# Kernel optimization log

Hardware: AMD Instinct MI355X
Metric: run time of the kernel (lower is better)

Reference implementation:

```python
import jax, jax.numpy as jnp
import numpy as np

B, NQ, NKV = 16, 4096, 77
QUERY_DIM, CONTEXT_DIM = 320, 768
HEADS, DIM_HEAD = 8, 64
INNER = HEADS * DIM_HEAD
SCALE = DIM_HEAD ** (-0.5)
MAX_NEG = -jnp.finfo(jnp.float32).max / 2


def setup_inputs() -> dict:
    key = jax.random.key(0)
    ks = jax.random.split(key, 8)
    x = jax.random.normal(ks[0], (B, NQ, QUERY_DIM), dtype=jnp.float32)
    context = jax.random.normal(ks[1], (B, NKV, CONTEXT_DIM), dtype=jnp.float32)
    mask = jax.random.randint(ks[2], (B, 1, 1, NKV), 0, 2).astype(bool)
    s = 0.02
    Wq = jax.random.normal(ks[3], (QUERY_DIM, INNER), dtype=jnp.float32) * s
    Wk = jax.random.normal(ks[4], (CONTEXT_DIM, INNER), dtype=jnp.float32) * s
    Wv = jax.random.normal(ks[5], (CONTEXT_DIM, INNER), dtype=jnp.float32) * s
    Wo = jax.random.normal(ks[6], (INNER, QUERY_DIM), dtype=jnp.float32) * s
    bo = jnp.zeros((QUERY_DIM,), dtype=jnp.float32)
    return {"x": x, "context": context, "mask": mask,
            "Wq": Wq, "Wk": Wk, "Wv": Wv, "Wo": Wo, "bo": bo}


def reference(x, context, mask, Wq, Wk, Wv, Wo, bo):
    # projections (bias-free Linears)
    q = (x @ Wq).reshape(B, NQ, HEADS, DIM_HEAD)        # b q h d
    k = (context @ Wk).reshape(B, NKV, HEADS, DIM_HEAD)  # b k h d
    v = (context @ Wv).reshape(B, NKV, HEADS, DIM_HEAD)  # b k h d
    # additive mask bias: 0 where mask, -finfo.max/2 where ~mask (matches masked_fill_)
    bias = jnp.where(mask, jnp.float32(0), MAX_NEG)      # broadcast to b h q k
    sim = jnp.einsum('bqhd,bkhd->bhqk', q, k) * SCALE + bias
    attn = jax.nn.softmax(sim, axis=-1)
    out = jnp.einsum('bhqk,bkhd->bqhd', attn, v).reshape(B, NQ, INNER)
    return out @ Wo + bo  # dropout p=0 -> identity
```

## Files before the change

### kernel.cpp

```cpp
#include <hip/hip_runtime.h>

typedef unsigned short ushort_t;
typedef __attribute__((ext_vector_type(8))) short bf16x8;
typedef __attribute__((ext_vector_type(4))) float f32x4;

#define B_SZ   16
#define NQ     4096
#define NKV    77
#define QDIM   320
#define CDIM   768
#define HEADS  8
#define DHEAD  64
#define INNER  512
#define M_ROWS (B_SZ * NQ)
#define VT_STR 104

__device__ __forceinline__ ushort_t f2bf(float f) {
  unsigned u = __builtin_bit_cast(unsigned, f);
  u = (u + 0x7fffu + ((u >> 16) & 1u)) >> 16;
  return (ushort_t)u;
}

__device__ __forceinline__ void async16(const ushort_t* g, ushort_t* l) {
  __builtin_amdgcn_global_load_lds(
      (const __attribute__((address_space(1))) unsigned int*)g,
      (__attribute__((address_space(3))) unsigned int*)l,
      16, 0, 0);
}

__global__ void mask_bias_kernel(const unsigned char* __restrict__ mraw,
                                 float* __restrict__ biasT) {
  __shared__ int s_u8, s_w4;
  if (threadIdx.x == 0) { s_u8 = 0; s_w4 = 0; }
  __syncthreads();
  const int nbytes = B_SZ * NKV;
  for (int i = threadIdx.x; i < nbytes; i += blockDim.x) {
    unsigned char v = mraw[i];
    if (v && (i & 3)) atomicOr(&s_u8, 1);
    if (v && ((i & 7) == 4)) atomicOr(&s_w4, 1);
  }
  __syncthreads();
  int mode = s_u8 ? 0 : (s_w4 ? 1 : 2);
  for (int i = threadIdx.x; i < B_SZ * 80; i += blockDim.x) {
    int b = i / 80, kv = i - b * 80;
    float bias = -2e30f;
    if (kv < NKV) {
      int idx = b * NKV + kv;
      long long m;
      if (mode == 0)      m = (long long)mraw[idx];
      else if (mode == 1) m = (long long)((const int*)mraw)[idx];
      else                m = ((const long long*)mraw)[idx];
      bias = m ? 0.0f : -1e30f;
    }
    biasT[i] = bias;
  }
}

__global__ void cast_f32_bf16(const float* __restrict__ in,
                              ushort_t* __restrict__ out, int n4) {
  int i = blockIdx.x * blockDim.x + threadIdx.x;
  int stride = gridDim.x * blockDim.x;
  const float4* in4 = (const float4*)in;
  ushort4* out4 = (ushort4*)out;
  for (; i < n4; i += stride) {
    float4 v = in4[i];
    ushort4 o;
    o.x = f2bf(v.x); o.y = f2bf(v.y); o.z = f2bf(v.z); o.w = f2bf(v.w);
    out4[i] = o;
  }
}

__global__ void tcast_f32_bf16(const float* __restrict__ in,
                               ushort_t* __restrict__ out,
                               int K, int N, int Npad, float scale) {
  int i = blockIdx.x * blockDim.x + threadIdx.x;
  int stride = gridDim.x * blockDim.x;
  int total = Npad * K;
  for (; i < total; i += stride) {
    int n = i / K, k = i - n * K;
    out[i] = (n < N) ? f2bf(in[(size_t)k * N + n] * scale) : (ushort_t)0;
  }
}

__global__ void vtrans_kernel(const ushort_t* __restrict__ kvb,
                              ushort_t* __restrict__ vt) {
  const int h = blockIdx.y, b = blockIdx.z;
  const int wid = threadIdx.x >> 6, lane = threadIdx.x & 63;
  const int d = blockIdx.x * 4 + wid;
  ushort_t* dst = vt + (size_t)(b * HEADS + h) * (64 * VT_STR) + d * VT_STR;
  for (int kv = lane; kv < VT_STR; kv += 64)
    dst[kv] = (kv < NKV)
        ? kvb[(size_t)(b * NKV + kv) * 1024 + 512 + h * 64 + d]
        : (ushort_t)0;
}

__global__ __launch_bounds__(256) void gemm_bf16(
    const ushort_t* __restrict__ A, const ushort_t* __restrict__ Bt,
    ushort_t* __restrict__ Cb, float* __restrict__ Cf,
    const float* __restrict__ bias,
    int K, int Astride, int Bstride, int Cstride, int Nvalid) {
  __shared__ ushort_t As[128 * 64];
  __shared__ ushort_t Bs[128 * 64];
  const int tid = threadIdx.x;
  const int wid = tid >> 6, lane = tid & 63;
  const int wr = wid >> 1, wc = wid & 1;
  const int tileM = blockIdx.x * 128, tileN = blockIdx.y * 128;

  f32x4 acc[4][4];
#pragma unroll
  for (int m = 0; m < 4; ++m)
#pragma unroll
    for (int n = 0; n < 4; ++n) acc[m][n] = (f32x4){0.f, 0.f, 0.f, 0.f};

  const int srow = lane >> 3;
  const int scol = (lane & 7) * 8;

  for (int kt = 0; kt < K; kt += 64) {
    __syncthreads();
#pragma unroll
    for (int j = 0; j < 4; ++j) {
      int s = wid * 4 + j;
      const ushort_t* ga = A + (size_t)(tileM + s * 8 + srow) * Astride + kt + scol;
      const ushort_t* gb = Bt + (size_t)(tileN + s * 8 + srow) * Bstride + kt + scol;
      async16(ga, As + s * 512);
      async16(gb, Bs + s * 512);
    }
    __syncthreads();
#pragma unroll
    for (int kc = 0; kc < 2; ++kc) {
      bf16x8 af[4], bfr[4];
#pragma unroll
      for (int m = 0; m < 4; ++m)
        af[m] = *(const bf16x8*)&As[(wr * 64 + m * 16 + (lane & 15)) * 64 + kc * 32 + (lane >> 4) * 8];
#pragma unroll
      for (int n = 0; n < 4; ++n)
        bfr[n] = *(const bf16x8*)&Bs[(wc * 64 + n * 16 + (lane & 15)) * 64 + kc * 32 + (lane >> 4) * 8];
#pragma unroll
      for (int m = 0; m < 4; ++m)
#pragma unroll
        for (int n = 0; n < 4; ++n)
          acc[m][n] = __builtin_amdgcn_mfma_f32_16x16x32_bf16(af[m], bfr[n], acc[m][n], 0, 0, 0);
    }
  }

  const int r0 = tileM + wr * 64;
  const int c0 = tileN + wc * 64;
  const int rl2 = (lane >> 4) * 4;
  const int cl = lane & 15;
  if (Cf) {
#pragma unroll
    for (int m = 0; m < 4; ++m)
#pragma unroll
      for (int n = 0; n < 4; ++n) {
        int col = c0 + n * 16 + cl;
        if (col < Nvalid) {
          float bv = bias ? bias[col] : 0.f;
#pragma unroll
          for (int r = 0; r < 4; ++r)
            Cf[(size_t)(r0 + m * 16 + rl2 + r) * Cstride + col] = acc[m][n][r] + bv;
        }
      }
  } else {
#pragma unroll
    for (int m = 0; m < 4; ++m)
#pragma unroll
      for (int n = 0; n < 4; ++n) {
        int col = c0 + n * 16 + cl;
#pragma unroll
        for (int r = 0; r < 4; ++r)
          Cb[(size_t)(r0 + m * 16 + rl2 + r) * Cstride + col] = f2bf(acc[m][n][r]);
      }
  }
}

__global__ __launch_bounds__(256) void attn_kernel(
    const ushort_t* __restrict__ qb, const ushort_t* __restrict__ kvb,
    const ushort_t* __restrict__ vt, const float* __restrict__ biasT,
    ushort_t* __restrict__ ab) {
  __shared__ ushort_t Vt[64 * VT_STR];
  __shared__ ushort_t P[4 * 16 * VT_STR];
  const int qt = blockIdx.x, h = blockIdx.y, b = blockIdx.z;
  const int tid = threadIdx.x, wid = tid >> 6, lane = tid & 63;
  const int rl = lane & 15;
  const int kh = (lane >> 4) * 8;

  const ushort_t* vtg = vt + (size_t)(b * HEADS + h) * (64 * VT_STR);
  for (int i = tid; i < 832; i += 256) async16(vtg + i * 8, Vt + i * 8);
  for (int i = tid; i < 832; i += 256)
    *(bf16x8*)&P[i * 8] = (bf16x8){0, 0, 0, 0, 0, 0, 0, 0};

  bf16x8 kf[5][2];
  float bias_v[5];
#pragma unroll
  for (int nt = 0; nt < 5; ++nt) {
    int kv = nt * 16 + rl;
    bias_v[nt] = biasT[b * 80 + kv];
    kf[nt][0] = (bf16x8){0, 0, 0, 0, 0, 0, 0, 0};
    kf[nt][1] = (bf16x8){0, 0, 0, 0, 0, 0, 0, 0};
    if (kv < NKV) {
      const ushort_t* kp = &kvb[(size_t)(b * NKV + kv) * 1024 + h * 64 + kh];
      kf[nt][0] = *(const bf16x8*)kp;
      kf[nt][1] = *(const bf16x8*)(kp + 32);
    }
  }
  __syncthreads();

  const int qbase = b * NQ + qt * 256;
  const int pbase = wid * (16 * VT_STR);
#pragma unroll 1
  for (int chunk = 0; chunk < 4; ++chunk) {
    if (chunk) __syncthreads();
    const int row0 = chunk * 64 + wid * 16;

    const ushort_t* qp = &qb[(size_t)(qbase + row0 + rl) * INNER + h * 64 + kh];
    bf16x8 qf0 = *(const bf16x8*)qp;
    bf16x8 qf1 = *(const bf16x8*)(qp + 32);

    f32x4 s[5];
#pragma unroll
    for (int nt = 0; nt < 5; ++nt) {
      s[nt] = (f32x4){0.f, 0.f, 0.f, 0.f};
      s[nt] = __builtin_amdgcn_mfma_f32_16x16x32_bf16(qf0, kf[nt][0], s[nt], 0, 0, 0);
      s[nt] = __builtin_amdgcn_mfma_f32_16x16x32_bf16(qf1, kf[nt][1], s[nt], 0, 0, 0);
    }

    float mx[4] = {-3.0e38f, -3.0e38f, -3.0e38f, -3.0e38f};
#pragma unroll
    for (int nt = 0; nt < 5; ++nt)
#pragma unroll
      for (int r = 0; r < 4; ++r) {
        float v = s[nt][r] + bias_v[nt];
        s[nt][r] = v;
        mx[r] = fmaxf(mx[r], v);
      }
#pragma unroll
    for (int d = 1; d < 16; d <<= 1)
#pragma unroll
      for (int r = 0; r < 4; ++r) mx[r] = fmaxf(mx[r], __shfl_xor(mx[r], d, 64));

    float sm[4] = {0.f, 0.f, 0.f, 0.f};
#pragma unroll
    for (int nt = 0; nt < 5; ++nt)
#pragma unroll
      for (int r = 0; r < 4; ++r) {
        float p = __expf(s[nt][r] - mx[r]);
        s[nt][r] = p;
        sm[r] += p;
      }
#pragma unroll
    for (int d = 1; d < 16; d <<= 1)
#pragma unroll
      for (int r = 0; r < 4; ++r) sm[r] += __shfl_xor(sm[r], d, 64);

    float rcp[4];
#pragma unroll
    for (int r = 0; r < 4; ++r) rcp[r] = 1.0f / sm[r];

#pragma unroll
    for (int nt = 0; nt < 5; ++nt)
#pragma unroll
      for (int r = 0; r < 4; ++r)
        P[pbase + ((lane >> 4) * 4 + r) * VT_STR + nt * 16 + rl] = f2bf(s[nt][r]);

    f32x4 o[4];
#pragma unroll
    for (int n = 0; n < 4; ++n) o[n] = (f32x4){0.f, 0.f, 0.f, 0.f};
#pragma unroll
    for (int kc = 0; kc < 3; ++kc) {
      bf16x8 pf = *(const bf16x8*)&P[pbase + rl * VT_STR + kc * 32 + kh];
#pragma unroll
      for (int n = 0; n < 4; ++n) {
        bf16x8 vf = *(const bf16x8*)&Vt[(n * 16 + rl) * VT_STR + kc * 32 + kh];
        o[n] = __builtin_amdgcn_mfma_f32_16x16x32_bf16(pf, vf, o[n], 0, 0, 0);
      }
    }

#pragma unroll
    for (int n = 0; n < 4; ++n)
#pragma unroll
      for (int r = 0; r < 4; ++r)
        P[pbase + ((lane >> 4) * 4 + r) * VT_STR + n * 16 + rl] = f2bf(o[n][r] * rcp[r]);

    __syncthreads();

    {
      const int rflat = tid >> 2, d0 = (tid & 3) * 16;
      const ushort_t* src = &P[(rflat >> 4) * (16 * VT_STR) + (rflat & 15) * VT_STR + d0];
      ushort_t* dst = &ab[(size_t)(qbase + chunk * 64 + rflat) * INNER + h * 64 + d0];
      *(bf16x8*)dst = *(const bf16x8*)src;
      *(bf16x8*)(dst + 8) = *(const bf16x8*)(src + 8);
    }
  }
}

extern "C" void kernel_launch(void* const* d_in, const int* in_sizes, int n_in,
                              void* d_out, int out_size, void* d_ws, size_t ws_size,
                              hipStream_t stream) {
  (void)in_sizes; (void)n_in; (void)out_size; (void)ws_size;
  const float* x   = (const float*)d_in[0];
  const float* ctx = (const float*)d_in[1];
  const unsigned char* mask = (const unsigned char*)d_in[2];
  const float* Wq = (const float*)d_in[3];
  const float* Wk = (const float*)d_in[4];
  const float* Wv = (const float*)d_in[5];
  const float* Wo = (const float*)d_in[6];
  const float* bo = (const float*)d_in[7];
  float* out = (float*)d_out;

  char* ws = (char*)d_ws;
  size_t off = 0;
  auto alloc = [&](size_t bytes) {
    char* p = ws + off;
    off += (bytes + 255) & ~(size_t)255;
    return p;
  };
  float*    biasT   = (float*)alloc(B_SZ * 80 * sizeof(float));
  ushort_t* region1 = (ushort_t*)alloc((size_t)M_ROWS * INNER * 2);
  ushort_t* xb = region1;
  ushort_t* ab = region1;
  ushort_t* qb   = (ushort_t*)alloc((size_t)M_ROWS * INNER * 2);
  ushort_t* cb   = (ushort_t*)alloc((size_t)1280 * CDIM * 2);
  ushort_t* Wqb  = (ushort_t*)alloc((size_t)INNER * QDIM * 2);
  ushort_t* Wkvb = (ushort_t*)alloc((size_t)1024 * CDIM * 2);
  ushort_t* Wob  = (ushort_t*)alloc((size_t)384 * INNER * 2);
  ushort_t* kvb  = (ushort_t*)alloc((size_t)1280 * 1024 * 2);
  ushort_t* vt   = (ushort_t*)alloc((size_t)B_SZ * HEADS * 64 * VT_STR * 2);

  mask_bias_kernel<<<1, 256, 0, stream>>>(mask, biasT);
  cast_f32_bf16<<<2048, 256, 0, stream>>>(x, xb, M_ROWS * QDIM / 4);
  cast_f32_bf16<<<512, 256, 0, stream>>>(ctx, cb, B_SZ * NKV * CDIM / 4);
  tcast_f32_bf16<<<640, 256, 0, stream>>>(Wq, Wqb, QDIM, INNER, INNER, 0.125f);
  tcast_f32_bf16<<<1536, 256, 0, stream>>>(Wk, Wkvb, CDIM, INNER, INNER, 1.0f);
  tcast_f32_bf16<<<1536, 256, 0, stream>>>(Wv, Wkvb + (size_t)INNER * CDIM, CDIM, INNER, INNER, 1.0f);
  tcast_f32_bf16<<<768, 256, 0, stream>>>(Wo, Wob, INNER, QDIM, 384, 1.0f);

  dim3 g1(M_ROWS / 128, INNER / 128);
  gemm_bf16<<<g1, 256, 0, stream>>>(xb, Wqb, qb, nullptr, nullptr,
                                    QDIM, QDIM, QDIM, INNER, INNER);
  dim3 g2(1280 / 128, 1024 / 128);
  gemm_bf16<<<g2, 256, 0, stream>>>(cb, Wkvb, kvb, nullptr, nullptr,
                                    CDIM, CDIM, CDIM, 1024, 1024);
  vtrans_kernel<<<dim3(16, HEADS, B_SZ), 256, 0, stream>>>(kvb, vt);
  attn_kernel<<<dim3(NQ / 256, HEADS, B_SZ), 256, 0, stream>>>(qb, kvb, vt, biasT, ab);
  dim3 g3(M_ROWS / 128, 384 / 128);
  gemm_bf16<<<g3, 256, 0, stream>>>(ab, Wob, nullptr, out, bo,
                                    INNER, INNER, INNER, QDIM, QDIM);
}
```

Before: 223.8 us.

## Fuse x cast into Q projection GEMM and add full-width double-buffered proj GEMMs

Removes the separate fp32-to-bf16 cast of x. The Q projection GEMM now reads fp32 x directly, converts it in registers and writes it into LDS, using a 128x512 tile so each A block is read once. The output projection gets its own 128x384 tile kernel with double-buffered async loads and the bias fused in. This cuts a full pass over the activations and the redundant re-reads of A across N tiles, at the cost of larger LDS use and more register pressure per block.

```diff
diff --git a/kernel.cpp b/kernel.cpp
--- a/kernel.cpp
+++ b/kernel.cpp
@@ -96,9 +96,8 @@
 
 __global__ __launch_bounds__(256) void gemm_bf16(
     const ushort_t* __restrict__ A, const ushort_t* __restrict__ Bt,
-    ushort_t* __restrict__ Cb, float* __restrict__ Cf,
-    const float* __restrict__ bias,
-    int K, int Astride, int Bstride, int Cstride, int Nvalid) {
+    ushort_t* __restrict__ Cb,
+    int K, int Astride, int Bstride, int Cstride) {
   __shared__ ushort_t As[128 * 64];
   __shared__ ushort_t Bs[128 * 64];
   const int tid = threadIdx.x;
@@ -147,29 +146,170 @@
   const int c0 = tileN + wc * 64;
   const int rl2 = (lane >> 4) * 4;
   const int cl = lane & 15;
-  if (Cf) {
+#pragma unroll
+  for (int m = 0; m < 4; ++m)
+#pragma unroll
+    for (int n = 0; n < 4; ++n) {
+      int col = c0 + n * 16 + cl;
+#pragma unroll
+      for (int r = 0; r < 4; ++r)
+        Cb[(size_t)(r0 + m * 16 + rl2 + r) * Cstride + col] = f2bf(acc[m][n][r]);
+    }
+}
+
+__global__ __launch_bounds__(512, 2) void gemm_qproj(
+    const float* __restrict__ x, const ushort_t* __restrict__ Wt,
+    ushort_t* __restrict__ qb) {
+  __shared__ ushort_t As[2][128 * 32];
+  __shared__ ushort_t Bs[2][512 * 32];
+  const int tid = threadIdx.x;
+  const int wid = tid >> 6, lane = tid & 63;
+  const int wr = wid & 1, wc = wid >> 1;
+  const int rl = lane & 15, kh = (lane >> 4) * 8;
+  const int tileM = blockIdx.x * 128;
+
+  f32x4 acc[4][8];
+#pragma unroll
+  for (int m = 0; m < 4; ++m)
+#pragma unroll
+    for (int n = 0; n < 8; ++n) acc[m][n] = (f32x4){0.f, 0.f, 0.f, 0.f};
+
+  const int arow = tid >> 3;
+  const int ac4 = tid & 7;
+  const float4* x4 = (const float4*)x;
+  float4 pa0, pa1;
+
+#define QP_ISSUE_A(KT)                                                        \
+  {                                                                           \
+    size_t base = (size_t)(tileM + arow) * 80 + ((KT) >> 2) + ac4;            \
+    pa0 = x4[base];                                                           \
+    pa1 = x4[base + (size_t)64 * 80];                                         \
+  }
+#define QP_WRITE_A(BUF)                                                       \
+  {                                                                           \
+    ushort4 u0, u1;                                                           \
+    u0.x = f2bf(pa0.x); u0.y = f2bf(pa0.y); u0.z = f2bf(pa0.z); u0.w = f2bf(pa0.w); \
+    u1.x = f2bf(pa1.x); u1.y = f2bf(pa1.y); u1.z = f2bf(pa1.z); u1.w = f2bf(pa1.w); \
+    *(ushort4*)&As[BUF][arow * 32 + ac4 * 4] = u0;                            \
+    *(ushort4*)&As[BUF][(arow + 64) * 32 + ac4 * 4] = u1;                     \
+  }
+#define QP_STAGE_B(BUF, KT)                                                   \
+  _Pragma("unroll")                                                           \
+  for (int i = 0; i < 4; ++i) {                                               \
+    int chunk = tid + i * 512;                                                \
+    int n = chunk >> 2, c8 = chunk & 3;                                       \
+    async16(Wt + (size_t)n * QDIM + (KT) + c8 * 8, &Bs[BUF][chunk * 8]);      \
+  }
+
+  QP_ISSUE_A(0)
+  QP_WRITE_A(0)
+  QP_STAGE_B(0, 0)
+  __syncthreads();
+
+  for (int s = 0; s < 10; ++s) {
+    const int cur = s & 1;
+    if (s < 9) {
+      QP_ISSUE_A((s + 1) * 32)
+      QP_STAGE_B(cur ^ 1, (s + 1) * 32)
+    }
+    bf16x8 af[4], bfr[8];
 #pragma unroll
     for (int m = 0; m < 4; ++m)
-#pragma unroll
-      for (int n = 0; n < 4; ++n) {
-        int col = c0 + n * 16 + cl;
-        if (col < Nvalid) {
-          float bv = bias ? bias[col] : 0.f;
-#pragma unroll
-          for (int r = 0; r < 4; ++r)
-            Cf[(size_t)(r0 + m * 16 + rl2 + r) * Cstride + col] = acc[m][n][r] + bv;
-        }
-      }
-  } else {
+      af[m] = *(const bf16x8*)&As[cur][(wr * 64 + m * 16 + rl) * 32 + kh];
+#pragma unroll
+    for (int n = 0; n < 8; ++n)
+      bfr[n] = *(const bf16x8*)&Bs[cur][(wc * 128 + n * 16 + rl) * 32 + kh];
 #pragma unroll
     for (int m = 0; m < 4; ++m)
 #pragma unroll
-      for (int n = 0; n < 4; ++n) {
-        int col = c0 + n * 16 + cl;
+      for (int n = 0; n < 8; ++n)
+        acc[m][n] = __builtin_amdgcn_mfma_f32_16x16x32_bf16(af[m], bfr[n], acc[m][n], 0, 0, 0);
+    if (s < 9) QP_WRITE_A(cur ^ 1)
+    __syncthreads();
+  }
+
+  const int r0 = tileM + wr * 64;
+  const int c0 = wc * 128;
+  const int rl2 = (lane >> 4) * 4, cl = lane & 15;
+#pragma unroll
+  for (int m = 0; m < 4; ++m)
+#pragma unroll
+    for (int n = 0; n < 8; ++n)
+#pragma unroll
+      for (int r = 0; r < 4; ++r)
+        qb[(size_t)(r0 + m * 16 + rl2 + r) * INNER + c0 + n * 16 + cl] = f2bf(acc[m][n][r]);
+}
+
+__global__ __launch_bounds__(512, 2) void gemm_oproj(
+    const ushort_t* __restrict__ A, const ushort_t* __restrict__ Wt,
+    const float* __restrict__ bo, float* __restrict__ out) {
+  __shared__ ushort_t As[2][128 * 64];
+  __shared__ ushort_t Bs[2][384 * 64];
+  const int tid = threadIdx.x;
+  const int wid = tid >> 6, lane = tid & 63;
+  const int wr = wid & 1, wc = wid >> 1;
+  const int rl = lane & 15, kh = (lane >> 4) * 8;
+  const int tileM = blockIdx.x * 128;
+
+  f32x4 acc[4][6];
+#pragma unroll
+  for (int m = 0; m < 4; ++m)
+#pragma unroll
+    for (int n = 0; n < 6; ++n) acc[m][n] = (f32x4){0.f, 0.f, 0.f, 0.f};
+
+#define OP_STAGE(BUF, KT)                                                     \
+  _Pragma("unroll")                                                           \
+  for (int i = 0; i < 2; ++i) {                                               \
+    int chunk = tid + i * 512;                                                \
+    int row = chunk >> 3, c8 = chunk & 7;                                     \
+    async16(A + (size_t)(tileM + row) * INNER + (KT) + c8 * 8,                \
+            &As[BUF][chunk * 8]);                                             \
+  }                                                                           \
+  _Pragma("unroll")                                                           \
+  for (int i = 0; i < 6; ++i) {                                               \
+    int chunk = tid + i * 512;                                                \
+    int n = chunk >> 3, c8 = chunk & 7;                                       \
+    async16(Wt + (size_t)n * INNER + (KT) + c8 * 8, &Bs[BUF][chunk * 8]);     \
+  }
+
+  OP_STAGE(0, 0)
+  __syncthreads();
+
+  for (int s = 0; s < 8; ++s) {
+    const int cur = s & 1;
+    if (s < 7) { OP_STAGE(cur ^ 1, (s + 1) * 64) }
+#pragma unroll
+    for (int kc = 0; kc < 2; ++kc) {
+      bf16x8 af[4], bfr[6];
+#pragma unroll
+      for (int m = 0; m < 4; ++m)
+        af[m] = *(const bf16x8*)&As[cur][(wr * 64 + m * 16 + rl) * 64 + kc * 32 + kh];
+#pragma unroll
+      for (int n = 0; n < 6; ++n)
+        bfr[n] = *(const bf16x8*)&Bs[cur][(wc * 96 + n * 16 + rl) * 64 + kc * 32 + kh];
+#pragma unroll
+      for (int m = 0; m < 4; ++m)
+#pragma unroll
+        for (int n = 0; n < 6; ++n)
+          acc[m][n] = __builtin_amdgcn_mfma_f32_16x16x32_bf16(af[m], bfr[n], acc[m][n], 0, 0, 0);
+    }
+    __syncthreads();
+  }
+
+  const int r0 = tileM + wr * 64;
+  const int c0 = wc * 96;
+  const int rl2 = (lane >> 4) * 4, cl = lane & 15;
+#pragma unroll
+  for (int n = 0; n < 6; ++n) {
+    int col = c0 + n * 16 + cl;
+    if (col < QDIM) {
+      float bv = bo[col];
+#pragma unroll
+      for (int m = 0; m < 4; ++m)
 #pragma unroll
         for (int r = 0; r < 4; ++r)
-          Cb[(size_t)(r0 + m * 16 + rl2 + r) * Cstride + col] = f2bf(acc[m][n][r]);
-      }
+          out[(size_t)(r0 + m * 16 + rl2 + r) * QDIM + col] = acc[m][n][r] + bv;
+    }
   }
 }
 
@@ -314,35 +454,27 @@
     off += (bytes + 255) & ~(size_t)255;
     return p;
   };
-  float*    biasT   = (float*)alloc(B_SZ * 80 * sizeof(float));
-  ushort_t* region1 = (ushort_t*)alloc((size_t)M_ROWS * INNER * 2);
-  ushort_t* xb = region1;
-  ushort_t* ab = region1;
-  ushort_t* qb   = (ushort_t*)alloc((size_t)M_ROWS * INNER * 2);
-  ushort_t* cb   = (ushort_t*)alloc((size_t)1280 * CDIM * 2);
-  ushort_t* Wqb  = (ushort_t*)alloc((size_t)INNER * QDIM * 2);
-  ushort_t* Wkvb = (ushort_t*)alloc((size_t)1024 * CDIM * 2);
-  ushort_t* Wob  = (ushort_t*)alloc((size_t)384 * INNER * 2);
-  ushort_t* kvb  = (ushort_t*)alloc((size_t)1280 * 1024 * 2);
-  ushort_t* vt   = (ushort_t*)alloc((size_t)B_SZ * HEADS * 64 * VT_STR * 2);
+  float*    biasT = (float*)alloc(B_SZ * 80 * sizeof(float));
+  ushort_t* ab    = (ushort_t*)alloc((size_t)M_ROWS * INNER * 2);
+  ushort_t* qb    = (ushort_t*)alloc((size_t)M_ROWS * INNER * 2);
+  ushort_t* cb    = (ushort_t*)alloc((size_t)1280 * CDIM * 2);
+  ushort_t* Wqb   = (ushort_t*)alloc((size_t)INNER * QDIM * 2);
+  ushort_t* Wkvb  = (ushort_t*)alloc((size_t)1024 * CDIM * 2);
+  ushort_t* Wob   = (ushort_t*)alloc((size_t)384 * INNER * 2);
+  ushort_t* kvb   = (ushort_t*)alloc((size_t)1280 * 1024 * 2);
+  ushort_t* vt    = (ushort_t*)alloc((size_t)B_SZ * HEADS * 64 * VT_STR * 2);
 
   mask_bias_kernel<<<1, 256, 0, stream>>>(mask, biasT);
-  cast_f32_bf16<<<2048, 256, 0, stream>>>(x, xb, M_ROWS * QDIM / 4);
   cast_f32_bf16<<<512, 256, 0, stream>>>(ctx, cb, B_SZ * NKV * CDIM / 4);
   tcast_f32_bf16<<<640, 256, 0, stream>>>(Wq, Wqb, QDIM, INNER, INNER, 0.125f);
   tcast_f32_bf16<<<1536, 256, 0, stream>>>(Wk, Wkvb, CDIM, INNER, INNER, 1.0f);
   tcast_f32_bf16<<<1536, 256, 0, stream>>>(Wv, Wkvb + (size_t)INNER * CDIM, CDIM, INNER, INNER, 1.0f);
   tcast_f32_bf16<<<768, 256, 0, stream>>>(Wo, Wob, INNER, QDIM, 384, 1.0f);
 
-  dim3 g1(M_ROWS / 128, INNER / 128);
-  gemm_bf16<<<g1, 256, 0, stream>>>(xb, Wqb, qb, nullptr, nullptr,
-                                    QDIM, QDIM, QDIM, INNER, INNER);
+  gemm_qproj<<<M_ROWS / 128, 512, 0, stream>>>(x, Wqb, qb);
   dim3 g2(1280 / 128, 1024 / 128);
-  gemm_bf16<<<g2, 256, 0, stream>>>(cb, Wkvb, kvb, nullptr, nullptr,
-                                    CDIM, CDIM, CDIM, 1024, 1024);
+  gemm_bf16<<<g2, 256, 0, stream>>>(cb, Wkvb, kvb, CDIM, CDIM, CDIM, 1024);
   vtrans_kernel<<<dim3(16, HEADS, B_SZ), 256, 0, stream>>>(kvb, vt);
   attn_kernel<<<dim3(NQ / 256, HEADS, B_SZ), 256, 0, stream>>>(qb, kvb, vt, biasT, ab);
-  dim3 g3(M_ROWS / 128, 384 / 128);
-  gemm_bf16<<<g3, 256, 0, stream>>>(ab, Wob, nullptr, out, bo,
-                                    INNER, INNER, INNER, QDIM, QDIM);
-}
+  gemm_oproj<<<M_ROWS / 128, 512, 0, stream>>>(ab, Wob, bo, out);
+}
```

Result: faster. 191.9 us (-14.2%).
